# Kernel optimization log

Hardware: AMD Instinct MI355X
Metric: run time of the kernel (lower is better)

## Reference

```python
import jax, jax.numpy as jnp
import numpy as np

B, T, N, H = 32, 512, 32, 128  # batch, time, num_series (== num_chans), hidden


def setup_inputs() -> dict:
    key = jax.random.key(0)
    ks = jax.random.split(key, 7)
    s = 1.0 / np.sqrt(H)  # PyTorch LSTM default init range
    X = jax.random.normal(ks[0], (B, T, N), dtype=jnp.float32)
    W_ih = jax.random.uniform(ks[1], (N, 4 * H, N), minval=-s, maxval=s, dtype=jnp.float32)
    W_hh = jax.random.uniform(ks[2], (N, 4 * H, H), minval=-s, maxval=s, dtype=jnp.float32)
    b_ih = jax.random.uniform(ks[3], (N, 4 * H), minval=-s, maxval=s, dtype=jnp.float32)
    b_hh = jax.random.uniform(ks[4], (N, 4 * H), minval=-s, maxval=s, dtype=jnp.float32)
    W_out = jax.random.uniform(ks[5], (N, H), minval=-s, maxval=s, dtype=jnp.float32)  # Conv1d(hidden,1,1) weight per series
    b_out = jax.random.uniform(ks[6], (N,), minval=-s, maxval=s, dtype=jnp.float32)
    return dict(X=X, W_ih=W_ih, W_hh=W_hh, b_ih=b_ih, b_hh=b_hh, W_out=W_out, b_out=b_out)


def reference(X, W_ih, W_hh, b_ih, b_hh, W_out, b_out):
    """Ensemble of N independent single-layer LSTMs over the same input X,
    each followed by a 1x1 conv (linear) head; outputs concatenated on dim 2.
    Gate order follows PyTorch: i, f, g, o."""
    Bsz, Tlen, P = X.shape
    Nser, _, Hid = W_hh.shape
    # Precompute input projections for all series/timesteps: [T, N, B, 4H]
    xproj = jnp.einsum('btp,ngp->tnbg', X, W_ih) + (b_ih + b_hh)[None, :, None, :]
    h0 = jnp.zeros((Nser, Bsz, Hid), X.dtype)
    c0 = jnp.zeros((Nser, Bsz, Hid), X.dtype)

    def step(carry, xt):
        h, c = carry
        gates = xt + jnp.einsum('nbh,ngh->nbg', h, W_hh)  # [N,B,4H]
        i, f, g, o = jnp.split(gates, 4, axis=-1)
        c = jax.nn.sigmoid(f) * c + jax.nn.sigmoid(i) * jnp.tanh(g)
        h = jax.nn.sigmoid(o) * jnp.tanh(c)
        return (h, c), h

    (hT, cT), hs = jax.lax.scan(step, (h0, c0), xproj)  # hs: [T, N, B, H]
    # 1x1 conv head per series, then concatenate along series dim -> [B, T, N]
    pred = jnp.einsum('tnbh,nh->btn', hs, W_out) + b_out[None, None, :]
    return pred, hT, cT
```

## Files before the change

### kernel.cpp

```cpp
#include <hip/hip_runtime.h>
#include <hip/hip_bf16.h>

typedef __attribute__((ext_vector_type(8))) short s16x8;
typedef __attribute__((ext_vector_type(4))) float f32x4;

#define MFMA_B16(a, b, c) __builtin_amdgcn_mfma_f32_16x16x32_bf16((a), (b), (c), 0, 0, 0)

static __device__ __forceinline__ short f2bf(float f) {
    __hip_bfloat16 h = __float2bfloat16(f);
    return __builtin_bit_cast(short, h);
}
static __device__ __forceinline__ float rcp_f(float x) {
    return __builtin_amdgcn_rcpf(x);
}

__global__ void xcvt_kernel(const float* __restrict__ X, short* __restrict__ Xb, int n) {
    int i = (blockIdx.x * 256 + threadIdx.x) * 4;
    if (i < n) {
        float4 v = *(const float4*)(X + i);
        short4 o;
        o.x = f2bf(v.x); o.y = f2bf(v.y); o.z = f2bf(v.z); o.w = f2bf(v.w);
        *(short4*)(Xb + i) = o;
    }
}

template<bool BF16X>
__global__ __launch_bounds__(512, 2)
void clstm_kernel(const float* __restrict__ X,
                  const short* __restrict__ Xb,
                  const float* __restrict__ W_ih,
                  const float* __restrict__ W_hh,
                  const float* __restrict__ b_ih,
                  const float* __restrict__ b_hh,
                  const float* __restrict__ W_out,
                  const float* __restrict__ b_out,
                  float* __restrict__ out)
{
    constexpr int B = 32, T = 512, N = 32, H = 128, G = 512;
    constexpr int HT_OFF = B * T * N;
    constexpr int CT_OFF = HT_OFF + N * B * H;
    constexpr int PRED_OFF = 8192;
    constexpr float C1 = 1.4426950408889634f;

    __shared__ __align__(16) unsigned char smem[16384];

    const int tid  = threadIdx.x;
    const int w    = tid >> 6;
    const int L    = tid & 63;
    const int col  = L & 15;
    const int quad = L >> 4;
    const int n    = blockIdx.x & 31;
    const int bgrp = blockIdx.x >> 5;

    s16x8 Bh[4][4];
    s16x8 Bx[4];
    f32x4 biasv[4];
#pragma unroll
    for (int tt = 0; tt < 4; ++tt) {
        const int g = (w + 8 * tt) * 16 + col;
        const float* whr = W_hh + ((size_t)n * G + g) * H + quad * 8;
#pragma unroll
        for (int kt = 0; kt < 4; ++kt) {
            const float* p = whr + kt * 32;
#pragma unroll
            for (int jj = 0; jj < 8; ++jj) Bh[tt][kt][jj] = f2bf(p[jj]);
        }
        const float* wir = W_ih + ((size_t)n * G + g) * N + quad * 8;
#pragma unroll
        for (int jj = 0; jj < 8; ++jj) Bx[tt][jj] = f2bf(wir[jj]);
        const float bb = b_ih[n * G + g] + b_hh[n * G + g];
        biasv[tt] = (f32x4){bb, bb, bb, bb};
    }

    s16x8 Bp[4];
    const float bo = b_out[n];
    const f32x4 bov = (f32x4){bo, bo, bo, bo};
#pragma unroll
    for (int kt = 0; kt < 4; ++kt) {
        const float* wp = W_out + n * H + kt * 32 + quad * 8;
#pragma unroll
        for (int jj = 0; jj < 8; ++jj)
            Bp[kt][jj] = (col == 0) ? f2bf(wp[jj]) : (short)0;
    }

    int wboff;
    {
        const int j = w * 16 + col;
        wboff = (j >> 5) * 1024 + (((((j >> 3) & 3) << 4) | (quad << 2)) * 16) + (j & 7) * 2;
    }

    const bool xactive = (col & 3) == 0;
    const int  xb      = bgrp * 4 + (col >> 2);
    const float* xp  = X + ((size_t)xb * T) * N + quad * 8;
    const short* xbp = BF16X ? (Xb + ((size_t)xb * T) * N + quad * 8) : nullptr;

    *(float4*)(smem + tid * 16)        = make_float4(0.f, 0.f, 0.f, 0.f);
    *(float4*)(smem + 8192 + tid * 16) = make_float4(0.f, 0.f, 0.f, 0.f);

    float cst = 0.f, hlast = 0.f;

    auto loadx = [&](int t) -> s16x8 {
        s16x8 r = (s16x8)(short)0;
        if (xactive) {
            if constexpr (BF16X) {
                r = *(const s16x8*)(xbp + (size_t)t * N);
            } else {
                float4 lo = *(const float4*)(xp + (size_t)t * N);
                float4 hi = *(const float4*)(xp + (size_t)t * N + 4);
                r[0] = f2bf(lo.x); r[1] = f2bf(lo.y); r[2] = f2bf(lo.z); r[3] = f2bf(lo.w);
                r[4] = f2bf(hi.x); r[5] = f2bf(hi.y); r[6] = f2bf(hi.z); r[7] = f2bf(hi.w);
            }
        }
        return r;
    };

    s16x8 xA, xB;
    {
        s16x8 x0 = loadx(0);
        xA = loadx(1);
        xB = loadx(2);
    }
    f32x4 accN[4];
    {
        s16x8 x0 = loadx(0);
#pragma unroll
        for (int tt = 0; tt < 4; ++tt)
            accN[tt] = MFMA_B16(x0, Bx[tt], biasv[tt]);
    }

    __syncthreads();

#define STEP(P, TCUR)                                                               \
    {                                                                               \
        const unsigned char* rb = smem + (P) * 4096;                                \
        s16x8 Af[4];                                                                \
        _Pragma("unroll")                                                           \
        for (int kt = 0; kt < 4; ++kt)                                              \
            Af[kt] = *(const s16x8*)(rb + kt * 1024 + L * 16);                      \
        f32x4 acc[4];                                                               \
        _Pragma("unroll")                                                           \
        for (int tt = 0; tt < 4; ++tt) acc[tt] = accN[tt];                          \
        _Pragma("unroll")                                                           \
        for (int kt = 0; kt < 4; ++kt) {                                            \
            _Pragma("unroll")                                                       \
            for (int tt = 0; tt < 4; ++tt)                                          \
                acc[tt] = MFMA_B16(Af[kt], Bh[tt][kt], acc[tt]);                    \
        }                                                                           \
        if (w == ((TCUR) & 7)) {                                                    \
            f32x4 pacc = bov;                                                       \
            _Pragma("unroll")                                                       \
            for (int kt = 0; kt < 4; ++kt)                                          \
                pacc = MFMA_B16(Af[kt], Bp[kt], pacc);                              \
            if ((TCUR) > 0 && col == 0)                                             \
                *(float*)(smem + PRED_OFF + ((quad << 9) + (TCUR) - 1) * 4) =       \
                    pacc[0];                                                        \
        }                                                                           \
                         \
        _Pragma("unroll")                                                           \
        for (int tt = 0; tt < 4; ++tt)                                              \
            accN[tt] = MFMA_B16(xA, Bx[tt], biasv[tt]);                             \
        xA = xB;                                                                    \
        xB = loadx(((TCUR) + 3 < T) ? (TCUR) + 3 : T - 1);                          \
                                     \
        {                                                                           \
            const float iv = acc[0][0], fv = acc[1][0];                             \
            const float gv = acc[2][0], ov = acc[3][0];                             \
            const float ei = exp2f(-C1 * iv);                                       \
            const float ef = exp2f(-C1 * fv);                                       \
            const float eg = exp2f(-2.0f * C1 * gv);                                \
            const float eo = exp2f(-C1 * ov);                                       \
            const float sf = rcp_f(1.0f + ef);                                      \
            const float itg = (1.0f - eg) * rcp_f((1.0f + ei) * (1.0f + eg));       \
            const float cc = __builtin_fmaf(sf, cst, itg);                          \
            cst = cc;                                                               \
            const float ec = exp2f(-2.0f * C1 * cc);                                \
            const float hv = (1.0f - ec) * rcp_f((1.0f + eo) * (1.0f + ec));        \
            hlast = hv;                                                             \
            *(short*)(smem + ((P) ^ 1) * 4096 + wboff) = f2bf(hv);                  \
        }                                                                           \
        __syncthreads();                                                            \
    }

#pragma unroll 1
    for (int t2 = 0; t2 < T; t2 += 2) {
        STEP(0, t2)
        STEP(1, t2 + 1)
    }
#undef STEP

    if (w == 0) {
        f32x4 pacc = bov;
#pragma unroll
        for (int kt = 0; kt < 4; ++kt) {
            s16x8 Af = *(const s16x8*)(smem + kt * 1024 + L * 16);
            pacc = MFMA_B16(Af, Bp[kt], pacc);
        }
        if (col == 0)
            *(float*)(smem + PRED_OFF + ((quad << 9) + (T - 1)) * 4) = pacc[0];
    }
    __syncthreads();

#pragma unroll
    for (int e = tid; e < 4 * T; e += 512) {
        const int b = e >> 9, t = e & (T - 1);
        out[((size_t)(bgrp * 4 + b) * T + t) * N + n] =
            *(const float*)(smem + PRED_OFF + e * 4);
    }

    {
        const int bglob = bgrp * 4 + quad;
        const int j = w * 16 + col;
        out[HT_OFF + ((size_t)n * B + bglob) * H + j] = hlast;
        out[CT_OFF + ((size_t)n * B + bglob) * H + j] = cst;
    }
}

extern "C" void kernel_launch(void* const* d_in, const int* in_sizes, int n_in,
                              void* d_out, int out_size, void* d_ws, size_t ws_size,
                              hipStream_t stream) {
    const float* X     = (const float*)d_in[0];
    const float* W_ih  = (const float*)d_in[1];
    const float* W_hh  = (const float*)d_in[2];
    const float* b_ih  = (const float*)d_in[3];
    const float* b_hh  = (const float*)d_in[4];
    const float* W_out = (const float*)d_in[5];
    const float* b_out = (const float*)d_in[6];
    float* out = (float*)d_out;

    const int xelems = 32 * 512 * 32;
    const bool usebf = ws_size >= (size_t)xelems * sizeof(short);

    if (usebf) {
        short* Xb = (short*)d_ws;
        xcvt_kernel<<<dim3(xelems / 1024), dim3(256), 0, stream>>>(X, Xb, xelems);
        clstm_kernel<true><<<dim3(256), dim3(512), 0, stream>>>(
            X, Xb, W_ih, W_hh, b_ih, b_hh, W_out, b_out, out);
    } else {
        clstm_kernel<false><<<dim3(256), dim3(512), 0, stream>>>(
            X, nullptr, W_ih, W_hh, b_ih, b_hh, W_out, b_out, out);
    }
}
```

Measured before the change: 366.0 us.

## Compute input projection for two timesteps per MFMA and defer head off critical path

Packs two consecutive timesteps into one MFMA for the input projection, using lanes col&1 to select the time offset. It computes the projection once every two steps and takes the second timestep's result from the accumulator's lane 1. The input projection is also folded into the first recurrent MFMA as its accumulator. The output-head MFMA is delayed by one step using saved A fragments, so it overlaps with later work instead of sitting on the serial recurrence path. This cuts wasted MFMA and load work but adds registers and a more involved indexing scheme.

```diff
diff --git a/kernel.cpp b/kernel.cpp
--- a/kernel.cpp
+++ b/kernel.cpp
@@ -89,78 +89,93 @@
         wboff = (j >> 5) * 1024 + (((((j >> 3) & 3) << 4) | (quad << 2)) * 16) + (j & 7) * 2;
     }
 
-    const bool xactive = (col & 3) == 0;
-    const int  xb      = bgrp * 4 + (col >> 2);
+    const int  xb  = bgrp * 4 + (col >> 2);
     const float* xp  = X + ((size_t)xb * T) * N + quad * 8;
     const short* xbp = BF16X ? (Xb + ((size_t)xb * T) * N + quad * 8) : nullptr;
+    const int toff = col & 1;
+
+    auto loadpair = [&](int tbase) -> s16x8 {
+        int t = tbase + toff; t = t < T ? t : T - 1;
+        if constexpr (BF16X) {
+            return *(const s16x8*)(xbp + (size_t)t * N);
+        } else {
+            float4 lo = *(const float4*)(xp + (size_t)t * N);
+            float4 hi = *(const float4*)(xp + (size_t)t * N + 4);
+            s16x8 r;
+            r[0] = f2bf(lo.x); r[1] = f2bf(lo.y); r[2] = f2bf(lo.z); r[3] = f2bf(lo.w);
+            r[4] = f2bf(hi.x); r[5] = f2bf(hi.y); r[6] = f2bf(hi.z); r[7] = f2bf(hi.w);
+            return r;
+        }
+    };
 
     *(float4*)(smem + tid * 16)        = make_float4(0.f, 0.f, 0.f, 0.f);
     *(float4*)(smem + 8192 + tid * 16) = make_float4(0.f, 0.f, 0.f, 0.f);
 
     float cst = 0.f, hlast = 0.f;
 
-    auto loadx = [&](int t) -> s16x8 {
-        s16x8 r = (s16x8)(short)0;
-        if (xactive) {
-            if constexpr (BF16X) {
-                r = *(const s16x8*)(xbp + (size_t)t * N);
-            } else {
-                float4 lo = *(const float4*)(xp + (size_t)t * N);
-                float4 hi = *(const float4*)(xp + (size_t)t * N + 4);
-                r[0] = f2bf(lo.x); r[1] = f2bf(lo.y); r[2] = f2bf(lo.z); r[3] = f2bf(lo.w);
-                r[4] = f2bf(hi.x); r[5] = f2bf(hi.y); r[6] = f2bf(hi.z); r[7] = f2bf(hi.w);
-            }
-        }
-        return r;
-    };
-
-    s16x8 xA, xB;
-    {
-        s16x8 x0 = loadx(0);
-        xA = loadx(1);
-        xB = loadx(2);
-    }
     f32x4 accN[4];
     {
-        s16x8 x0 = loadx(0);
+        s16x8 p01 = loadpair(0);
 #pragma unroll
         for (int tt = 0; tt < 4; ++tt)
-            accN[tt] = MFMA_B16(x0, Bx[tt], biasv[tt]);
-    }
+            accN[tt] = MFMA_B16(p01, Bx[tt], biasv[tt]);
+    }
+    s16x8 xC = loadpair(2);
+    s16x8 xN = loadpair(4);
+    s16x8 Afs[4];
+    f32x4 Pq[4];
 
     __syncthreads();
 
-#define STEP(P, TCUR)                                                               \
+#define STEP(P, TCUR, ISODD)                                                        \
     {                                                                               \
         const unsigned char* rb = smem + (P) * 4096;                                \
         s16x8 Af[4];                                                                \
         _Pragma("unroll")                                                           \
         for (int kt = 0; kt < 4; ++kt)                                              \
             Af[kt] = *(const s16x8*)(rb + kt * 1024 + L * 16);                      \
+                       \
+        if (ISODD) {                                                                \
+            _Pragma("unroll")                                                       \
+            for (int tt = 0; tt < 4; ++tt)                                          \
+                Pq[tt] = MFMA_B16(xC, Bx[tt], biasv[tt]);                           \
+        }                                                                           \
+              \
+        if ((TCUR) > 1 && w == (((TCUR) - 1) & 7)) {                                \
+            f32x4 pacc = bov;                                                       \
+            _Pragma("unroll")                                                       \
+            for (int kt = 0; kt < 4; ++kt)                                          \
+                pacc = MFMA_B16(Afs[kt], Bp[kt], pacc);                             \
+            if (col == 0)                                                           \
+                *(float*)(smem + PRED_OFF + ((quad << 9) + (TCUR) - 2) * 4) =       \
+                    pacc[0];                                                        \
+        }                                                                           \
+                                                             \
         f32x4 acc[4];                                                               \
         _Pragma("unroll")                                                           \
-        for (int tt = 0; tt < 4; ++tt) acc[tt] = accN[tt];                          \
+        for (int tt = 0; tt < 4; ++tt)                                              \
+            acc[tt] = MFMA_B16(Af[0], Bh[tt][0], accN[tt]);                         \
         _Pragma("unroll")                                                           \
-        for (int kt = 0; kt < 4; ++kt) {                                            \
+        for (int kt = 1; kt < 4; ++kt) {                                            \
             _Pragma("unroll")                                                       \
             for (int tt = 0; tt < 4; ++tt)                                          \
                 acc[tt] = MFMA_B16(Af[kt], Bh[tt][kt], acc[tt]);                    \
         }                                                                           \
         if (w == ((TCUR) & 7)) {                                                    \
-            f32x4 pacc = bov;                                                       \
-            _Pragma("unroll")                                                       \
-            for (int kt = 0; kt < 4; ++kt)                                          \
-                pacc = MFMA_B16(Af[kt], Bp[kt], pacc);                              \
-            if ((TCUR) > 0 && col == 0)                                             \
-                *(float*)(smem + PRED_OFF + ((quad << 9) + (TCUR) - 1) * 4) =       \
-                    pacc[0];                                                        \
-        }                                                                           \
-                         \
-        _Pragma("unroll")                                                           \
-        for (int tt = 0; tt < 4; ++tt)                                              \
-            accN[tt] = MFMA_B16(xA, Bx[tt], biasv[tt]);                             \
-        xA = xB;                                                                    \
-        xB = loadx(((TCUR) + 3 < T) ? (TCUR) + 3 : T - 1);                          \
+            _Pragma("unroll")                                                       \
+            for (int kt = 0; kt < 4; ++kt) Afs[kt] = Af[kt];                        \
+        }                                                                           \
+                                             \
+        if (ISODD) {                                                                \
+            _Pragma("unroll")                                                       \
+            for (int tt = 0; tt < 4; ++tt) accN[tt] = Pq[tt];                       \
+            xC = xN;                                                                \
+            xN = loadpair((TCUR) + 5);                                              \
+        } else {                                                                    \
+            _Pragma("unroll")                                                       \
+            for (int tt = 0; tt < 4; ++tt)                                          \
+                accN[tt] = __builtin_shufflevector(acc[tt], acc[tt], 1, 1, 1, 1);   \
+        }                                                                           \
                                      \
         {                                                                           \
             const float iv = acc[0][0], fv = acc[1][0];                             \
@@ -183,11 +198,19 @@
 
 #pragma unroll 1
     for (int t2 = 0; t2 < T; t2 += 2) {
-        STEP(0, t2)
-        STEP(1, t2 + 1)
+        STEP(0, t2,     0)
+        STEP(1, t2 + 1, 1)
     }
 #undef STEP
 
+    if (w == ((T - 1) & 7)) {
+        f32x4 pacc = bov;
+#pragma unroll
+        for (int kt = 0; kt < 4; ++kt)
+            pacc = MFMA_B16(Afs[kt], Bp[kt], pacc);
+        if (col == 0)
+            *(float*)(smem + PRED_OFF + ((quad << 9) + (T - 2)) * 4) = pacc[0];
+    }
     if (w == 0) {
         f32x4 pacc = bov;
 #pragma unroll
```

New measurement: 373.3 us. About the same (+2.0%).
